# Optimization experiments

Hardware: AMD Instinct MI355X
Metric: run time of the kernel (lower is better)

The kernel has to match this reference:

```python
import jax, jax.numpy as jnp
import numpy as np

N_NODES = 100000
N_EDGES = 1600000
IN_CH = 1024
FEAT_CH = 128
OUT_CH = 3


def setup_inputs() -> dict:
    key = jax.random.key(0)
    ks = jax.random.split(key, 9)
    features = jax.random.normal(ks[0], (N_NODES, IN_CH), dtype=jnp.float32)
    edges = jax.random.randint(ks[1], (2, N_EDGES), 0, N_NODES, dtype=jnp.int64)
    edges2 = jax.random.randint(ks[2], (2, N_EDGES), 0, N_NODES, dtype=jnp.int64)
    edge_features = jax.random.normal(ks[3], (N_EDGES, 1), dtype=jnp.float32)
    additional_feature = jax.random.normal(ks[4], (N_NODES, 20), dtype=jnp.float32)
    # GCNConv linear weights (glorot-ish scale) and biases
    W1 = jax.random.normal(ks[5], (IN_CH, FEAT_CH), dtype=jnp.float32) * (1.0 / np.sqrt(IN_CH))
    b1 = jnp.zeros((FEAT_CH,), dtype=jnp.float32)
    W2 = jax.random.normal(ks[6], (FEAT_CH, OUT_CH), dtype=jnp.float32) * (1.0 / np.sqrt(FEAT_CH))
    b2 = jnp.zeros((OUT_CH,), dtype=jnp.float32)
    return {"features": features, "edges": edges, "edges2": edges2,
            "edge_features": edge_features, "additional_feature": additional_feature,
            "W1": W1, "b1": b1, "W2": W2, "b2": b2}


def gcn_conv(x, edge_index, W, b, num_nodes):
    """PyG GCNConv: x' = D^{-1/2}(A+I)D^{-1/2} x W + b (self-loops added)."""
    x = x @ W  # project first (cheaper feature dim for aggregation)
    loop = jnp.arange(num_nodes, dtype=edge_index.dtype)
    src = jnp.concatenate([edge_index[0], loop])
    dst = jnp.concatenate([edge_index[1], loop])
    deg = jax.ops.segment_sum(jnp.ones_like(dst, dtype=x.dtype), dst,
                              num_segments=num_nodes)  # >=1 due to self-loops
    dinv = jax.lax.rsqrt(deg)
    norm = dinv[src] * dinv[dst]  # [E+N]
    out = jax.ops.segment_sum(x[src] * norm[:, None], dst, num_segments=num_nodes)
    return out + b


def reference(features, edges, edges2, edge_features, additional_feature, W1, b1, W2, b2):
    # use_additional_channels=False -> features unchanged; edge_features forced to None
    n = features.shape[0]
    x = gcn_conv(features, edges2, W1, b1, n)
    x = jax.nn.relu(x)
    # dropout inactive in eval mode
    return gcn_conv(x, edges2, W2, b2, n)
```

## Files before the change

kernel.cpp:

```cpp
#include <hip/hip_runtime.h>
#include <hip/hip_bf16.h>

typedef __attribute__((ext_vector_type(8))) _Float16 half8;
typedef __attribute__((ext_vector_type(4))) float f32x4;

#define N_NODES 100000
#define N_EDGES 1600000
#define IN_CH 1024
#define FEAT 128
#define CAP 64
#define NDIG 196
#define CAPC 10240
#define NTILES ((N_NODES + 127) / 128)

__global__ void k_prep(const float* __restrict__ W1, _Float16* __restrict__ W1t,
                       int* __restrict__ cursorC, int* __restrict__ done) {
    int idx = blockIdx.x * 256 + threadIdx.x;
    if (idx < IN_CH * FEAT) {
        int col = idx & (FEAT - 1);
        int k = idx >> 7;
        W1t[(size_t)col * IN_CH + k] = (_Float16)W1[idx];
    }
    if (idx < NDIG) cursorC[idx] = idx * CAPC;
    if (idx == 0) *done = 0;
}

__global__ __launch_bounds__(256, 2) void k_build_gemm(
    const float* __restrict__ A, const _Float16* __restrict__ Bt,
    const int4* __restrict__ src4, const int4* __restrict__ dst4,
    int* __restrict__ cursorC, uint2* __restrict__ recs,
    int* __restrict__ csr, int* __restrict__ cnt, int* __restrict__ done,
    _Float16* __restrict__ H, int M, int e4)
{
    __shared__ union {
        _Float16 Bs[2][128][72];
        struct { int hist[NDIG], segoff[NDIG], lcur[NDIG]; } bin;
        int cl[512];
    } sm;
    const int t = threadIdx.x;

    if (blockIdx.x < NDIG) {
        const int b = blockIdx.x;
        if (t < NDIG) sm.bin.hist[t] = 0;
        __syncthreads();

        const int base4 = b * 2048;
        int4 sv[8], dv[8];
#pragma unroll
        for (int j = 0; j < 8; ++j) {
            int idx = base4 + j * 256 + t;
            if (idx < e4) { sv[j] = src4[idx]; dv[j] = dst4[idx]; }
            else { sv[j] = (int4){-1,-1,-1,-1}; dv[j] = (int4){-1,-1,-1,-1}; }
        }
#pragma unroll
        for (int j = 0; j < 8; ++j) {
            int dd[4] = {dv[j].x, dv[j].y, dv[j].z, dv[j].w};
            int ss[4] = {sv[j].x, sv[j].y, sv[j].z, sv[j].w};
#pragma unroll
            for (int c = 0; c < 4; ++c)
                if ((unsigned)dd[c] < N_NODES && (unsigned)ss[c] < N_NODES)
                    atomicAdd(&sm.bin.hist[dd[c] >> 9], 1);
        }
        __syncthreads();
        if (t < NDIG) {
            sm.bin.segoff[t] = atomicAdd(&cursorC[t], sm.bin.hist[t]);
            sm.bin.lcur[t] = 0;
        }
        __syncthreads();
#pragma unroll
        for (int j = 0; j < 8; ++j) {
            int dd[4] = {dv[j].x, dv[j].y, dv[j].z, dv[j].w};
            int ss[4] = {sv[j].x, sv[j].y, sv[j].z, sv[j].w};
#pragma unroll
            for (int c = 0; c < 4; ++c) {
                if ((unsigned)dd[c] < N_NODES && (unsigned)ss[c] < N_NODES) {
                    int dg = dd[c] >> 9;
                    int r = atomicAdd(&sm.bin.lcur[dg], 1);
                    int pos = sm.bin.segoff[dg] + r;
                    if (pos < (dg + 1) * CAPC)
                        recs[pos] = (uint2){(unsigned)ss[c], (unsigned)dd[c]};
                }
            }
        }
        __syncthreads();
        if (t == 0) {
            __threadfence();
            __hip_atomic_fetch_add(done, 1, __ATOMIC_RELEASE, __HIP_MEMORY_SCOPE_AGENT);
            while (__hip_atomic_load(done, __ATOMIC_ACQUIRE, __HIP_MEMORY_SCOPE_AGENT) < NDIG)
                __builtin_amdgcn_s_sleep(8);
        }
        __syncthreads();
        const int d = blockIdx.x;
        for (int j = t; j < 512; j += 256) sm.cl[j] = 0;
        __syncthreads();
        const int base = d * CAPC;
        int n = cursorC[d] - base;
        if (n > CAPC) n = CAPC;
        for (int k = t; k < n; k += 256) {
            uint2 r = recs[base + k];
            int local = (int)r.y & 511;
            int slot = atomicAdd(&sm.cl[local], 1);
            if (slot < CAP) csr[((int)r.y << 6) + slot] = (int)r.x;
        }
        __syncthreads();
        const int node0 = d << 9;
        for (int j = t; j < 512; j += 256) {
            int node = node0 + j;
            if (node < N_NODES) cnt[node] = sm.cl[j] < CAP ? sm.cl[j] : CAP;
        }
        return;
    }

    const int wid = t >> 6, lane = t & 63;
    const int brow0 = (blockIdx.x - NDIG) * 128;
    const int NKT = IN_CH / 64;

    f32x4 acc[2][8];
#pragma unroll
    for (int m = 0; m < 2; ++m)
#pragma unroll
        for (int nn = 0; nn < 8; ++nn) acc[m][nn] = (f32x4){0.f, 0.f, 0.f, 0.f};

    int r0 = brow0 + wid * 32 + (lane & 15);
    int r1 = r0 + 16;
    if (r0 >= M) r0 = M - 1;
    if (r1 >= M) r1 = M - 1;
    const int kbase = (lane >> 4) * 8;
    const float* pa0 = A + (size_t)r0 * IN_CH + kbase;
    const float* pa1 = A + (size_t)r1 * IN_CH + kbase;
    const int bcol = t >> 1;
    const int bko = (t & 1) * 32;
    const _Float16* pb = Bt + (size_t)bcol * IN_CH + bko;

    float4 ar[2][2][2];
    half8 af[2][2];
    half8 bst[4];

#define LOAD_A(kt)                                                              \
    {                                                                           \
        _Pragma("unroll") for (int m = 0; m < 2; ++m) {                         \
            const float* p_ = (m ? pa1 : pa0) + (kt) * 64;                      \
            _Pragma("unroll") for (int kk = 0; kk < 2; ++kk) {                  \
                ar[m][kk][0] = *(const float4*)(p_ + kk * 32);                  \
                ar[m][kk][1] = *(const float4*)(p_ + kk * 32 + 4);              \
            }                                                                   \
        }                                                                       \
    }
#define CVT_A()                                                                 \
    {                                                                           \
        _Pragma("unroll") for (int m = 0; m < 2; ++m)                           \
        _Pragma("unroll") for (int kk = 0; kk < 2; ++kk) {                      \
            half8 h;                                                            \
            h[0] = (_Float16)ar[m][kk][0].x; h[1] = (_Float16)ar[m][kk][0].y;   \
            h[2] = (_Float16)ar[m][kk][0].z; h[3] = (_Float16)ar[m][kk][0].w;   \
            h[4] = (_Float16)ar[m][kk][1].x; h[5] = (_Float16)ar[m][kk][1].y;   \
            h[6] = (_Float16)ar[m][kk][1].z; h[7] = (_Float16)ar[m][kk][1].w;   \
            af[m][kk] = h;                                                      \
        }                                                                       \
    }
#define LOAD_B(kt)                                                              \
    {                                                                           \
        const half8* s_ = (const half8*)(pb + (kt) * 64);                       \
        _Pragma("unroll") for (int j = 0; j < 4; ++j) bst[j] = s_[j];           \
    }
#define WRITE_B(buf)                                                            \
    {                                                                           \
        _Pragma("unroll") for (int j = 0; j < 4; ++j)                           \
            *(half8*)(&sm.Bs[buf][bcol][bko + j * 8]) = bst[j];                 \
    }

    LOAD_A(0); LOAD_B(0);
    CVT_A();
    WRITE_B(0);
    __syncthreads();

    for (int kt = 0; kt < NKT; ++kt) {
        const int cur = kt & 1;
        const bool more = (kt + 1 < NKT);
        if (more) { LOAD_B(kt + 1); LOAD_A(kt + 1); }
#pragma unroll
        for (int kk = 0; kk < 2; ++kk) {
            half8 a0 = af[0][kk], a1 = af[1][kk];
#pragma unroll
            for (int nn = 0; nn < 8; ++nn) {
                half8 bb = *(const half8*)(&sm.Bs[cur][nn * 16 + (lane & 15)][kk * 32 + kbase]);
                acc[0][nn] = __builtin_amdgcn_mfma_f32_16x16x32_f16(a0, bb, acc[0][nn], 0, 0, 0);
                acc[1][nn] = __builtin_amdgcn_mfma_f32_16x16x32_f16(a1, bb, acc[1][nn], 0, 0, 0);
            }
        }
        if (more) {
            CVT_A();
            WRITE_B(cur ^ 1);
            __syncthreads();
        }
    }
#undef LOAD_A
#undef CVT_A
#undef LOAD_B
#undef WRITE_B

    int colb = lane & 15, rgrp = (lane >> 4) * 4;
#pragma unroll
    for (int m = 0; m < 2; ++m) {
#pragma unroll
        for (int r = 0; r < 4; ++r) {
            int grow = brow0 + wid * 32 + m * 16 + rgrp + r;
            if (grow < M) {
                _Float16* hp = H + (size_t)grow * FEAT + colb;
#pragma unroll
                for (int nn = 0; nn < 8; ++nn) hp[nn * 16] = (_Float16)acc[m][nn][r];
            }
        }
    }
}

__device__ __forceinline__ float dinv_of(const int* cnt, int i, int& m) {
    m = cnt[i];
    return rsqrtf((float)(m + 1));
}

__global__ __launch_bounds__(256) void k_agg1(const _Float16* __restrict__ H,
                                              const int* __restrict__ csr,
                                              const int* __restrict__ cnt,
                                              const float* __restrict__ b1,
                                              const float* __restrict__ W2,
                                              float* __restrict__ Y, int n) {
    int wid = threadIdx.x >> 6, lane = threadIdx.x & 63;
    int i = blockIdx.x * 4 + wid;
    if (i >= n) return;
    const int g = lane >> 4, u = lane & 15;
    int m;
    float di = dinv_of(cnt, i, m);
    int base = i << 6;

    int sl; float dl;
    if (lane < m) {
        sl = csr[base + lane];
        int cs = cnt[sl];
        dl = rsqrtf((float)(cs + 1));
    } else {
        sl = i;
        dl = (lane == m) ? di : 0.f;
    }
    int mm = (m < 63 ? m : 63) + 1;

    float ax[8];
#pragma unroll
    for (int j = 0; j < 8; ++j) ax[j] = 0.f;

    for (int e = 0; e < mm; e += 8) {
        int i0 = e + g, i1 = e + 4 + g;
        bool v0 = i0 < mm, v1 = i1 < mm;
        int c0i = v0 ? i0 : 0, c1i = v1 ? i1 : 0;
        int s0 = __shfl(sl, c0i);
        float w0 = __shfl(dl, c0i);
        int s1 = __shfl(sl, c1i);
        float w1 = __shfl(dl, c1i);
        if (!v0) { s0 = i; w0 = 0.f; }
        if (!v1) { s1 = i; w1 = 0.f; }
        half8 h0 = *(const half8*)(H + ((size_t)s0 << 7) + u * 8);
        half8 h1 = *(const half8*)(H + ((size_t)s1 << 7) + u * 8);
#pragma unroll
        for (int j = 0; j < 8; ++j) ax[j] += w0 * (float)h0[j] + w1 * (float)h1[j];
    }

#pragma unroll
    for (int j = 0; j < 8; ++j) {
        ax[j] += __shfl_xor(ax[j], 16);
        ax[j] += __shfl_xor(ax[j], 32);
    }

    int c0 = u * 8;
    float y0 = 0.f, y1 = 0.f, y2 = 0.f;
#pragma unroll
    for (int j = 0; j < 8; ++j) {
        float x = di * ax[j] + b1[c0 + j];
        x = x > 0.f ? x : 0.f;
        y0 += x * W2[(c0 + j) * 3 + 0];
        y1 += x * W2[(c0 + j) * 3 + 1];
        y2 += x * W2[(c0 + j) * 3 + 2];
    }
#pragma unroll
    for (int d = 1; d < 16; d <<= 1) {
        y0 += __shfl_xor(y0, d);
        y1 += __shfl_xor(y1, d);
        y2 += __shfl_xor(y2, d);
    }
    if (lane == 0) {
        float* yp = Y + (size_t)i * 4;
        yp[0] = di * y0; yp[1] = di * y1; yp[2] = di * y2;
    }
}

__global__ void k_agg2(const float* __restrict__ Y, const int* __restrict__ csr,
                       const int* __restrict__ cnt, const float* __restrict__ b2,
                       float* __restrict__ out, int n) {
    int i = blockIdx.x * 256 + threadIdx.x;
    if (i >= n) return;
    int m;
    float di = dinv_of(cnt, i, m);
    int base = i << 6;
    const float4* Y4 = (const float4*)Y;
    float4 self = Y4[i];
    float a0 = self.x, a1 = self.y, a2 = self.z;
    int e = 0;
    for (; e + 1 < m; e += 2) {
        int s0 = csr[base + e], s1 = csr[base + e + 1];
        float4 v0 = Y4[s0], v1 = Y4[s1];
        a0 += v0.x + v1.x;
        a1 += v0.y + v1.y;
        a2 += v0.z + v1.z;
    }
    if (e < m) {
        float4 v0 = Y4[csr[base + e]];
        a0 += v0.x; a1 += v0.y; a2 += v0.z;
    }
    out[(size_t)i * 3 + 0] = di * a0 + b2[0];
    out[(size_t)i * 3 + 1] = di * a1 + b2[1];
    out[(size_t)i * 3 + 2] = di * a2 + b2[2];
}

extern "C" void kernel_launch(void* const* d_in, const int* in_sizes, int n_in,
                              void* d_out, int out_size, void* d_ws, size_t ws_size,
                              hipStream_t stream) {
    const float* features = (const float*)d_in[0];
    const int* edges2 = (const int*)d_in[2];
    const float* W1 = (const float*)d_in[5];
    const float* b1 = (const float*)d_in[6];
    const float* W2 = (const float*)d_in[7];
    const float* b2 = (const float*)d_in[8];
    float* out = (float*)d_out;

    const int N = N_NODES, E = N_EDGES;
    const int* srcp = edges2;
    const int* dstp = edges2 + E;

    char* p = (char*)d_ws;
    auto carve = [&](size_t bytes) { char* q = p; p += (bytes + 255) & ~(size_t)255; return q; };
    int* cnt      = (int*)carve(4 * (size_t)N);
    int* cursorC  = (int*)carve(4 * NDIG);
    int* done     = (int*)carve(4);
    uint2* recs   = (uint2*)carve(8 * (size_t)NDIG * CAPC);
    int* csr      = (int*)carve(4 * (size_t)N * CAP);
    _Float16* W1t = (_Float16*)carve(2 * (size_t)IN_CH * FEAT);
    _Float16* H   = (_Float16*)carve(2 * (size_t)N * FEAT);
    float* Y      = (float*)carve(16 * (size_t)N);

    k_prep<<<dim3(512), dim3(256), 0, stream>>>(W1, W1t, cursorC, done);
    k_build_gemm<<<dim3(NDIG + NTILES), dim3(256), 0, stream>>>(
        features, W1t, (const int4*)srcp, (const int4*)dstp,
        cursorC, recs, csr, cnt, done, H, N, E / 4);
    k_agg1<<<dim3((N + 3) / 4), dim3(256), 0, stream>>>(H, csr, cnt, b1, W2, Y, N);
    k_agg2<<<dim3((N + 255) / 256), dim3(256), 0, stream>>>(Y, csr, cnt, b2, out, N);
}
```

Before: 269.5 us.

## Fuse all stages into one persistent cooperative kernel with grid syncs

Merges weight prep, CSR build, GEMM, and both aggregation stages into one cooperative persistent kernel. Stages are separated by grid.sync, and GEMM tiles are handed out through an atomic tile counter. Each agg1 wave prefetches the next node's count and neighbor list. This is meant to remove the overhead of four kernel launches and the gaps between them. The cost is that the grid is capped at 512 resident blocks, so the GEMM and aggregation run with fewer workers and pay for grid-wide barriers.

```diff
diff --git a/kernel.cpp b/kernel.cpp
--- a/kernel.cpp
+++ b/kernel.cpp
@@ -1,5 +1,8 @@
 #include <hip/hip_runtime.h>
 #include <hip/hip_bf16.h>
+#include <hip/hip_cooperative_groups.h>
+
+namespace cg = cooperative_groups;
 
 typedef __attribute__((ext_vector_type(8))) _Float16 half8;
 typedef __attribute__((ext_vector_type(4))) float f32x4;
@@ -13,12 +16,351 @@
 #define CAPC 10240
 #define NTILES ((N_NODES + 127) / 128)
 
+template <typename LDS>
+__device__ __forceinline__ void gemm_tile(LDS* Bs, const float* __restrict__ A,
+                                          const _Float16* __restrict__ Bt,
+                                          _Float16* __restrict__ H, int M,
+                                          int tile, int t) {
+    const int wid = t >> 6, lane = t & 63;
+    const int brow0 = tile * 128;
+    const int NKT = IN_CH / 64;
+
+    f32x4 acc[2][8];
+#pragma unroll
+    for (int m = 0; m < 2; ++m)
+#pragma unroll
+        for (int nn = 0; nn < 8; ++nn) acc[m][nn] = (f32x4){0.f, 0.f, 0.f, 0.f};
+
+    int r0 = brow0 + wid * 32 + (lane & 15);
+    int r1 = r0 + 16;
+    if (r0 >= M) r0 = M - 1;
+    if (r1 >= M) r1 = M - 1;
+    const int kbase = (lane >> 4) * 8;
+    const float* pa0 = A + (size_t)r0 * IN_CH + kbase;
+    const float* pa1 = A + (size_t)r1 * IN_CH + kbase;
+    const int bcol = t >> 1;
+    const int bko = (t & 1) * 32;
+    const _Float16* pb = Bt + (size_t)bcol * IN_CH + bko;
+
+    float4 ar[2][2][2];
+    half8 af[2][2];
+    half8 bst[4];
+
+#define LOAD_A(kt)                                                              \
+    {                                                                           \
+        _Pragma("unroll") for (int m = 0; m < 2; ++m) {                         \
+            const float* p_ = (m ? pa1 : pa0) + (kt) * 64;                      \
+            _Pragma("unroll") for (int kk = 0; kk < 2; ++kk) {                  \
+                ar[m][kk][0] = *(const float4*)(p_ + kk * 32);                  \
+                ar[m][kk][1] = *(const float4*)(p_ + kk * 32 + 4);              \
+            }                                                                   \
+        }                                                                       \
+    }
+#define CVT_A()                                                                 \
+    {                                                                           \
+        _Pragma("unroll") for (int m = 0; m < 2; ++m)                           \
+        _Pragma("unroll") for (int kk = 0; kk < 2; ++kk) {                      \
+            half8 h;                                                            \
+            h[0] = (_Float16)ar[m][kk][0].x; h[1] = (_Float16)ar[m][kk][0].y;   \
+            h[2] = (_Float16)ar[m][kk][0].z; h[3] = (_Float16)ar[m][kk][0].w;   \
+            h[4] = (_Float16)ar[m][kk][1].x; h[5] = (_Float16)ar[m][kk][1].y;   \
+            h[6] = (_Float16)ar[m][kk][1].z; h[7] = (_Float16)ar[m][kk][1].w;   \
+            af[m][kk] = h;                                                      \
+        }                                                                       \
+    }
+#define LOAD_B(kt)                                                              \
+    {                                                                           \
+        const half8* s_ = (const half8*)(pb + (kt) * 64);                       \
+        _Pragma("unroll") for (int j = 0; j < 4; ++j) bst[j] = s_[j];           \
+    }
+#define WRITE_B(buf)                                                            \
+    {                                                                           \
+        _Pragma("unroll") for (int j = 0; j < 4; ++j)                           \
+            *(half8*)(&(*Bs)[buf][bcol][bko + j * 8]) = bst[j];                 \
+    }
+
+    LOAD_A(0); LOAD_B(0);
+    CVT_A();
+    WRITE_B(0);
+    __syncthreads();
+
+    for (int kt = 0; kt < NKT; ++kt) {
+        const int cur = kt & 1;
+        const bool more = (kt + 1 < NKT);
+        if (more) { LOAD_B(kt + 1); LOAD_A(kt + 1); }
+#pragma unroll
+        for (int kk = 0; kk < 2; ++kk) {
+            half8 a0 = af[0][kk], a1 = af[1][kk];
+#pragma unroll
+            for (int nn = 0; nn < 8; ++nn) {
+                half8 bb = *(const half8*)(&(*Bs)[cur][nn * 16 + (lane & 15)][kk * 32 + kbase]);
+                acc[0][nn] = __builtin_amdgcn_mfma_f32_16x16x32_f16(a0, bb, acc[0][nn], 0, 0, 0);
+                acc[1][nn] = __builtin_amdgcn_mfma_f32_16x16x32_f16(a1, bb, acc[1][nn], 0, 0, 0);
+            }
+        }
+        if (more) {
+            CVT_A();
+            WRITE_B(cur ^ 1);
+            __syncthreads();
+        }
+    }
+#undef LOAD_A
+#undef CVT_A
+#undef LOAD_B
+#undef WRITE_B
+
+    int colb = lane & 15, rgrp = (lane >> 4) * 4;
+#pragma unroll
+    for (int m = 0; m < 2; ++m) {
+#pragma unroll
+        for (int r = 0; r < 4; ++r) {
+            int grow = brow0 + wid * 32 + m * 16 + rgrp + r;
+            if (grow < M) {
+                _Float16* hp = H + (size_t)grow * FEAT + colb;
+#pragma unroll
+                for (int nn = 0; nn < 8; ++nn) hp[nn * 16] = (_Float16)acc[m][nn][r];
+            }
+        }
+    }
+}
+
+__device__ __forceinline__ void agg1_node(const _Float16* __restrict__ H,
+                                          const int* __restrict__ cnt,
+                                          const float* __restrict__ b1,
+                                          const float* __restrict__ W2,
+                                          float* __restrict__ Y,
+                                          int i, int lane, int m, int sl_raw) {
+    const int g = lane >> 4, u = lane & 15;
+    float di = rsqrtf((float)(m + 1));
+    int sl; float dl;
+    if (lane < m) {
+        sl = sl_raw;
+        int cs = cnt[sl];
+        dl = rsqrtf((float)(cs + 1));
+    } else {
+        sl = i;
+        dl = (lane == m) ? di : 0.f;
+    }
+    int mm = (m < 63 ? m : 63) + 1;
+
+    float ax[8];
+#pragma unroll
+    for (int j = 0; j < 8; ++j) ax[j] = 0.f;
+
+    for (int e = 0; e < mm; e += 8) {
+        int i0 = e + g, i1 = e + 4 + g;
+        bool v0 = i0 < mm, v1 = i1 < mm;
+        int c0i = v0 ? i0 : 0, c1i = v1 ? i1 : 0;
+        int s0 = __shfl(sl, c0i);
+        float w0 = __shfl(dl, c0i);
+        int s1 = __shfl(sl, c1i);
+        float w1 = __shfl(dl, c1i);
+        if (!v0) { s0 = i; w0 = 0.f; }
+        if (!v1) { s1 = i; w1 = 0.f; }
+        half8 h0 = *(const half8*)(H + ((size_t)s0 << 7) + u * 8);
+        half8 h1 = *(const half8*)(H + ((size_t)s1 << 7) + u * 8);
+#pragma unroll
+        for (int j = 0; j < 8; ++j) ax[j] += w0 * (float)h0[j] + w1 * (float)h1[j];
+    }
+
+#pragma unroll
+    for (int j = 0; j < 8; ++j) {
+        ax[j] += __shfl_xor(ax[j], 16);
+        ax[j] += __shfl_xor(ax[j], 32);
+    }
+
+    int c0 = u * 8;
+    float y0 = 0.f, y1 = 0.f, y2 = 0.f;
+#pragma unroll
+    for (int j = 0; j < 8; ++j) {
+        float x = di * ax[j] + b1[c0 + j];
+        x = x > 0.f ? x : 0.f;
+        y0 += x * W2[(c0 + j) * 3 + 0];
+        y1 += x * W2[(c0 + j) * 3 + 1];
+        y2 += x * W2[(c0 + j) * 3 + 2];
+    }
+#pragma unroll
+    for (int d = 1; d < 16; d <<= 1) {
+        y0 += __shfl_xor(y0, d);
+        y1 += __shfl_xor(y1, d);
+        y2 += __shfl_xor(y2, d);
+    }
+    if (lane == 0) {
+        float* yp = Y + (size_t)i * 4;
+        yp[0] = di * y0; yp[1] = di * y1; yp[2] = di * y2;
+    }
+}
+
+__device__ __forceinline__ void agg2_node(const float* __restrict__ Y,
+                                          const int* __restrict__ csr,
+                                          const int* __restrict__ cnt,
+                                          const float* __restrict__ b2,
+                                          float* __restrict__ out, int i) {
+    int m = cnt[i];
+    float di = rsqrtf((float)(m + 1));
+    int base = i << 6;
+    const float4* Y4 = (const float4*)Y;
+    float4 self = Y4[i];
+    float a0 = self.x, a1 = self.y, a2 = self.z;
+    int e = 0;
+    for (; e + 1 < m; e += 2) {
+        int s0 = csr[base + e], s1 = csr[base + e + 1];
+        float4 v0 = Y4[s0], v1 = Y4[s1];
+        a0 += v0.x + v1.x;
+        a1 += v0.y + v1.y;
+        a2 += v0.z + v1.z;
+    }
+    if (e < m) {
+        float4 v0 = Y4[csr[base + e]];
+        a0 += v0.x; a1 += v0.y; a2 += v0.z;
+    }
+    out[(size_t)i * 3 + 0] = di * a0 + b2[0];
+    out[(size_t)i * 3 + 1] = di * a1 + b2[1];
+    out[(size_t)i * 3 + 2] = di * a2 + b2[2];
+}
+
+__global__ __launch_bounds__(256, 2) void k_mega(
+    const float* __restrict__ A, const float* __restrict__ W1,
+    const int4* __restrict__ src4, const int4* __restrict__ dst4,
+    const float* __restrict__ b1, const float* __restrict__ W2,
+    const float* __restrict__ b2, float* __restrict__ out,
+    int* __restrict__ cursorC, uint2* __restrict__ recs,
+    int* __restrict__ csr, int* __restrict__ cnt,
+    int* __restrict__ done, int* __restrict__ tilectr,
+    _Float16* __restrict__ W1t, _Float16* __restrict__ H,
+    float* __restrict__ Y, int e4)
+{
+    cg::grid_group grid = cg::this_grid();
+    __shared__ union {
+        _Float16 Bs[2][128][72];
+        struct { int hist[NDIG], segoff[NDIG], lcur[NDIG]; } bin;
+        int cl[512];
+    } sm;
+    const int t = threadIdx.x;
+    const int b = blockIdx.x;
+    const int nb = gridDim.x;
+    const int gtid = b * 256 + t;
+    const int nthr = nb * 256;
+
+    for (int idx = gtid; idx < IN_CH * FEAT; idx += nthr) {
+        int col = idx & (FEAT - 1), k = idx >> 7;
+        W1t[(size_t)col * IN_CH + k] = (_Float16)W1[idx];
+    }
+    if (gtid < NDIG) cursorC[gtid] = gtid * CAPC;
+    if (gtid == 0) { *done = 0; *tilectr = 0; }
+    grid.sync();
+
+    if (b < NDIG) {
+        if (t < NDIG) sm.bin.hist[t] = 0;
+        __syncthreads();
+        const int base4 = b * 2048;
+        int4 sv[8], dv[8];
+#pragma unroll
+        for (int j = 0; j < 8; ++j) {
+            int idx = base4 + j * 256 + t;
+            if (idx < e4) { sv[j] = src4[idx]; dv[j] = dst4[idx]; }
+            else { sv[j] = (int4){-1,-1,-1,-1}; dv[j] = (int4){-1,-1,-1,-1}; }
+        }
+#pragma unroll
+        for (int j = 0; j < 8; ++j) {
+            int dd[4] = {dv[j].x, dv[j].y, dv[j].z, dv[j].w};
+            int ss[4] = {sv[j].x, sv[j].y, sv[j].z, sv[j].w};
+#pragma unroll
+            for (int c = 0; c < 4; ++c)
+                if ((unsigned)dd[c] < N_NODES && (unsigned)ss[c] < N_NODES)
+                    atomicAdd(&sm.bin.hist[dd[c] >> 9], 1);
+        }
+        __syncthreads();
+        if (t < NDIG) {
+            sm.bin.segoff[t] = atomicAdd(&cursorC[t], sm.bin.hist[t]);
+            sm.bin.lcur[t] = 0;
+        }
+        __syncthreads();
+#pragma unroll
+        for (int j = 0; j < 8; ++j) {
+            int dd[4] = {dv[j].x, dv[j].y, dv[j].z, dv[j].w};
+            int ss[4] = {sv[j].x, sv[j].y, sv[j].z, sv[j].w};
+#pragma unroll
+            for (int c = 0; c < 4; ++c) {
+                if ((unsigned)dd[c] < N_NODES && (unsigned)ss[c] < N_NODES) {
+                    int dg = dd[c] >> 9;
+                    int r = atomicAdd(&sm.bin.lcur[dg], 1);
+                    int pos = sm.bin.segoff[dg] + r;
+                    if (pos < (dg + 1) * CAPC)
+                        recs[pos] = (uint2){(unsigned)ss[c], (unsigned)dd[c]};
+                }
+            }
+        }
+        __syncthreads();
+        if (t == 0) {
+            __threadfence();
+            __hip_atomic_fetch_add(done, 1, __ATOMIC_RELEASE, __HIP_MEMORY_SCOPE_AGENT);
+            while (__hip_atomic_load(done, __ATOMIC_ACQUIRE, __HIP_MEMORY_SCOPE_AGENT) < NDIG)
+                __builtin_amdgcn_s_sleep(8);
+        }
+        __syncthreads();
+        for (int j = t; j < 512; j += 256) sm.cl[j] = 0;
+        __syncthreads();
+        const int base = b * CAPC;
+        int n = cursorC[b] - base;
+        if (n > CAPC) n = CAPC;
+        for (int k = t; k < n; k += 256) {
+            uint2 r = recs[base + k];
+            int local = (int)r.y & 511;
+            int slot = atomicAdd(&sm.cl[local], 1);
+            if (slot < CAP) csr[((int)r.y << 6) + slot] = (int)r.x;
+        }
+        __syncthreads();
+        const int node0 = b << 9;
+        for (int j = t; j < 512; j += 256) {
+            int node = node0 + j;
+            if (node < N_NODES) cnt[node] = sm.cl[j] < CAP ? sm.cl[j] : CAP;
+        }
+    }
+    {
+        __shared__ int tsh;
+        for (;;) {
+            __syncthreads();
+            if (t == 0) tsh = atomicAdd(tilectr, 1);
+            __syncthreads();
+            int tile = tsh;
+            if (tile >= NTILES) break;
+            gemm_tile(&sm.Bs, A, W1t, H, N_NODES, tile, t);
+        }
+    }
+    grid.sync();
+
+    {
+        const int wid = t >> 6, lane = t & 63;
+        const int stride = nb * 4;
+        int i = b * 4 + wid;
+        int m_cur = 0, sl_cur = 0;
+        if (i < N_NODES) {
+            m_cur = cnt[i];
+            sl_cur = csr[(i << 6) + lane];
+        }
+        for (; i < N_NODES; ) {
+            int inext = i + stride;
+            int m_pf = 0, sl_pf = 0;
+            if (inext < N_NODES) {
+                m_pf = cnt[inext];
+                sl_pf = csr[(inext << 6) + lane];
+            }
+            agg1_node(H, cnt, b1, W2, Y, i, lane, m_cur, sl_cur);
+            i = inext; m_cur = m_pf; sl_cur = sl_pf;
+        }
+    }
+    grid.sync();
+
+    for (int i = gtid; i < N_NODES; i += nthr)
+        agg2_node(Y, csr, cnt, b2, out, i);
+}
+
 __global__ void k_prep(const float* __restrict__ W1, _Float16* __restrict__ W1t,
                        int* __restrict__ cursorC, int* __restrict__ done) {
     int idx = blockIdx.x * 256 + threadIdx.x;
     if (idx < IN_CH * FEAT) {
-        int col = idx & (FEAT - 1);
-        int k = idx >> 7;
+        int col = idx & (FEAT - 1), k = idx >> 7;
         W1t[(size_t)col * IN_CH + k] = (_Float16)W1[idx];
     }
     if (idx < NDIG) cursorC[idx] = idx * CAPC;
@@ -43,7 +385,6 @@
         const int b = blockIdx.x;
         if (t < NDIG) sm.bin.hist[t] = 0;
         __syncthreads();
-
         const int base4 = b * 2048;
         int4 sv[8], dv[8];
 #pragma unroll
@@ -90,11 +431,10 @@
                 __builtin_amdgcn_s_sleep(8);
         }
         __syncthreads();
-        const int d = blockIdx.x;
         for (int j = t; j < 512; j += 256) sm.cl[j] = 0;
         __syncthreads();
-        const int base = d * CAPC;
-        int n = cursorC[d] - base;
+        const int base = blockIdx.x * CAPC;
+        int n = cursorC[blockIdx.x] - base;
         if (n > CAPC) n = CAPC;
         for (int k = t; k < n; k += 256) {
             uint2 r = recs[base + k];
@@ -103,120 +443,14 @@
             if (slot < CAP) csr[((int)r.y << 6) + slot] = (int)r.x;
         }
         __syncthreads();
-        const int node0 = d << 9;
+        const int node0 = blockIdx.x << 9;
         for (int j = t; j < 512; j += 256) {
             int node = node0 + j;
             if (node < N_NODES) cnt[node] = sm.cl[j] < CAP ? sm.cl[j] : CAP;
         }
         return;
     }
-
-    const int wid = t >> 6, lane = t & 63;
-    const int brow0 = (blockIdx.x - NDIG) * 128;
-    const int NKT = IN_CH / 64;
-
-    f32x4 acc[2][8];
-#pragma unroll
-    for (int m = 0; m < 2; ++m)
-#pragma unroll
-        for (int nn = 0; nn < 8; ++nn) acc[m][nn] = (f32x4){0.f, 0.f, 0.f, 0.f};
-
-    int r0 = brow0 + wid * 32 + (lane & 15);
-    int r1 = r0 + 16;
-    if (r0 >= M) r0 = M - 1;
-    if (r1 >= M) r1 = M - 1;
-    const int kbase = (lane >> 4) * 8;
-    const float* pa0 = A + (size_t)r0 * IN_CH + kbase;
-    const float* pa1 = A + (size_t)r1 * IN_CH + kbase;
-    const int bcol = t >> 1;
-    const int bko = (t & 1) * 32;
-    const _Float16* pb = Bt + (size_t)bcol * IN_CH + bko;
-
-    float4 ar[2][2][2];
-    half8 af[2][2];
-    half8 bst[4];
-
-#define LOAD_A(kt)                                                              \
-    {                                                                           \
-        _Pragma("unroll") for (int m = 0; m < 2; ++m) {                         \
-            const float* p_ = (m ? pa1 : pa0) + (kt) * 64;                      \
-            _Pragma("unroll") for (int kk = 0; kk < 2; ++kk) {                  \
-                ar[m][kk][0] = *(const float4*)(p_ + kk * 32);                  \
-                ar[m][kk][1] = *(const float4*)(p_ + kk * 32 + 4);              \
-            }                                                                   \
-        }                                                                       \
-    }
-#define CVT_A()                                                                 \
-    {                                                                           \
-        _Pragma("unroll") for (int m = 0; m < 2; ++m)                           \
-        _Pragma("unroll") for (int kk = 0; kk < 2; ++kk) {                      \
-            half8 h;                                                            \
-            h[0] = (_Float16)ar[m][kk][0].x; h[1] = (_Float16)ar[m][kk][0].y;   \
-            h[2] = (_Float16)ar[m][kk][0].z; h[3] = (_Float16)ar[m][kk][0].w;   \
-            h[4] = (_Float16)ar[m][kk][1].x; h[5] = (_Float16)ar[m][kk][1].y;   \
-            h[6] = (_Float16)ar[m][kk][1].z; h[7] = (_Float16)ar[m][kk][1].w;   \
-            af[m][kk] = h;                                                      \
-        }                                                                       \
-    }
-#define LOAD_B(kt)                                                              \
-    {                                                                           \
-        const half8* s_ = (const half8*)(pb + (kt) * 64);                       \
-        _Pragma("unroll") for (int j = 0; j < 4; ++j) bst[j] = s_[j];           \
-    }
-#define WRITE_B(buf)                                                            \
-    {                                                                           \
-        _Pragma("unroll") for (int j = 0; j < 4; ++j)                           \
-            *(half8*)(&sm.Bs[buf][bcol][bko + j * 8]) = bst[j];                 \
-    }
-
-    LOAD_A(0); LOAD_B(0);
-    CVT_A();
-    WRITE_B(0);
-    __syncthreads();
-
-    for (int kt = 0; kt < NKT; ++kt) {
-        const int cur = kt & 1;
-        const bool more = (kt + 1 < NKT);
-        if (more) { LOAD_B(kt + 1); LOAD_A(kt + 1); }
-#pragma unroll
-        for (int kk = 0; kk < 2; ++kk) {
-            half8 a0 = af[0][kk], a1 = af[1][kk];
-#pragma unroll
-            for (int nn = 0; nn < 8; ++nn) {
-                half8 bb = *(const half8*)(&sm.Bs[cur][nn * 16 + (lane & 15)][kk * 32 + kbase]);
-                acc[0][nn] = __builtin_amdgcn_mfma_f32_16x16x32_f16(a0, bb, acc[0][nn], 0, 0, 0);
-                acc[1][nn] = __builtin_amdgcn_mfma_f32_16x16x32_f16(a1, bb, acc[1][nn], 0, 0, 0);
-            }
-        }
-        if (more) {
-            CVT_A();
-            WRITE_B(cur ^ 1);
-            __syncthreads();
-        }
-    }
-#undef LOAD_A
-#undef CVT_A
-#undef LOAD_B
-#undef WRITE_B
-
-    int colb = lane & 15, rgrp = (lane >> 4) * 4;
-#pragma unroll
-    for (int m = 0; m < 2; ++m) {
-#pragma unroll
-        for (int r = 0; r < 4; ++r) {
-            int grow = brow0 + wid * 32 + m * 16 + rgrp + r;
-            if (grow < M) {
-                _Float16* hp = H + (size_t)grow * FEAT + colb;
-#pragma unroll
-                for (int nn = 0; nn < 8; ++nn) hp[nn * 16] = (_Float16)acc[m][nn][r];
-            }
-        }
-    }
-}
-
-__device__ __forceinline__ float dinv_of(const int* cnt, int i, int& m) {
-    m = cnt[i];
-    return rsqrtf((float)(m + 1));
+    gemm_tile(&sm.Bs, A, Bt, H, M, blockIdx.x - NDIG, t);
 }
 
 __global__ __launch_bounds__(256) void k_agg1(const _Float16* __restrict__ H,
@@ -228,68 +462,9 @@
     int wid = threadIdx.x >> 6, lane = threadIdx.x & 63;
     int i = blockIdx.x * 4 + wid;
     if (i >= n) return;
-    const int g = lane >> 4, u = lane & 15;
-    int m;
-    float di = dinv_of(cnt, i, m);
-    int base = i << 6;
-
-    int sl; float dl;
-    if (lane < m) {
-        sl = csr[base + lane];
-        int cs = cnt[sl];
-        dl = rsqrtf((float)(cs + 1));
-    } else {
-        sl = i;
-        dl = (lane == m) ? di : 0.f;
-    }
-    int mm = (m < 63 ? m : 63) + 1;
-
-    float ax[8];
-#pragma unroll
-    for (int j = 0; j < 8; ++j) ax[j] = 0.f;
-
-    for (int e = 0; e < mm; e += 8) {
-        int i0 = e + g, i1 = e + 4 + g;
-        bool v0 = i0 < mm, v1 = i1 < mm;
-        int c0i = v0 ? i0 : 0, c1i = v1 ? i1 : 0;
-        int s0 = __shfl(sl, c0i);
-        float w0 = __shfl(dl, c0i);
-        int s1 = __shfl(sl, c1i);
-        float w1 = __shfl(dl, c1i);
-        if (!v0) { s0 = i; w0 = 0.f; }
-        if (!v1) { s1 = i; w1 = 0.f; }
-        half8 h0 = *(const half8*)(H + ((size_t)s0 << 7) + u * 8);
-        half8 h1 = *(const half8*)(H + ((size_t)s1 << 7) + u * 8);
-#pragma unroll
-        for (int j = 0; j < 8; ++j) ax[j] += w0 * (float)h0[j] + w1 * (float)h1[j];
-    }
-
-#pragma unroll
-    for (int j = 0; j < 8; ++j) {
-        ax[j] += __shfl_xor(ax[j], 16);
-        ax[j] += __shfl_xor(ax[j], 32);
-    }
-
-    int c0 = u * 8;
-    float y0 = 0.f, y1 = 0.f, y2 = 0.f;
-#pragma unroll
-    for (int j = 0; j < 8; ++j) {
-        float x = di * ax[j] + b1[c0 + j];
-        x = x > 0.f ? x : 0.f;
-        y0 += x * W2[(c0 + j) * 3 + 0];
-        y1 += x * W2[(c0 + j) * 3 + 1];
-        y2 += x * W2[(c0 + j) * 3 + 2];
-    }
-#pragma unroll
-    for (int d = 1; d < 16; d <<= 1) {
-        y0 += __shfl_xor(y0, d);
-        y1 += __shfl_xor(y1, d);
-        y2 += __shfl_xor(y2, d);
-    }
-    if (lane == 0) {
-        float* yp = Y + (size_t)i * 4;
-        yp[0] = di * y0; yp[1] = di * y1; yp[2] = di * y2;
-    }
+    int m = cnt[i];
+    int sl_raw = (lane < m) ? csr[(i << 6) + lane] : 0;
+    agg1_node(H, cnt, b1, W2, Y, i, lane, m, sl_raw);
 }
 
 __global__ void k_agg2(const float* __restrict__ Y, const int* __restrict__ csr,
@@ -297,27 +472,7 @@
                        float* __restrict__ out, int n) {
     int i = blockIdx.x * 256 + threadIdx.x;
     if (i >= n) return;
-    int m;
-    float di = dinv_of(cnt, i, m);
-    int base = i << 6;
-    const float4* Y4 = (const float4*)Y;
-    float4 self = Y4[i];
-    float a0 = self.x, a1 = self.y, a2 = self.z;
-    int e = 0;
-    for (; e + 1 < m; e += 2) {
-        int s0 = csr[base + e], s1 = csr[base + e + 1];
-        float4 v0 = Y4[s0], v1 = Y4[s1];
-        a0 += v0.x + v1.x;
-        a1 += v0.y + v1.y;
-        a2 += v0.z + v1.z;
-    }
-    if (e < m) {
-        float4 v0 = Y4[csr[base + e]];
-        a0 += v0.x; a1 += v0.y; a2 += v0.z;
-    }
-    out[(size_t)i * 3 + 0] = di * a0 + b2[0];
-    out[(size_t)i * 3 + 1] = di * a1 + b2[1];
-    out[(size_t)i * 3 + 2] = di * a2 + b2[2];
+    agg2_node(Y, csr, cnt, b2, out, i);
 }
 
 extern "C" void kernel_launch(void* const* d_in, const int* in_sizes, int n_in,
@@ -334,22 +489,43 @@
     const int N = N_NODES, E = N_EDGES;
     const int* srcp = edges2;
     const int* dstp = edges2 + E;
+    const int4* src4 = (const int4*)srcp;
+    const int4* dst4 = (const int4*)dstp;
+    int e4 = E / 4;
 
     char* p = (char*)d_ws;
     auto carve = [&](size_t bytes) { char* q = p; p += (bytes + 255) & ~(size_t)255; return q; };
     int* cnt      = (int*)carve(4 * (size_t)N);
     int* cursorC  = (int*)carve(4 * NDIG);
     int* done     = (int*)carve(4);
+    int* tilectr  = (int*)carve(4);
     uint2* recs   = (uint2*)carve(8 * (size_t)NDIG * CAPC);
     int* csr      = (int*)carve(4 * (size_t)N * CAP);
     _Float16* W1t = (_Float16*)carve(2 * (size_t)IN_CH * FEAT);
     _Float16* H   = (_Float16*)carve(2 * (size_t)N * FEAT);
     float* Y      = (float*)carve(16 * (size_t)N);
 
+    int dev = 0, ncu = 0, maxb = 0;
+    bool coop_ok = (hipGetDevice(&dev) == hipSuccess) &&
+                   (hipDeviceGetAttribute(&ncu, hipDeviceAttributeMultiprocessorCount, dev) == hipSuccess) &&
+                   (hipOccupancyMaxActiveBlocksPerMultiprocessor(&maxb, k_mega, 256, 0) == hipSuccess) &&
+                   maxb >= 1 && ncu >= 1;
+    int grid = coop_ok ? maxb * ncu : 0;
+    if (grid > 512) grid = 512;
+    if (coop_ok && grid >= NDIG + 4) {
+        void* args[] = {(void*)&features, (void*)&W1, (void*)&src4, (void*)&dst4,
+                        (void*)&b1, (void*)&W2, (void*)&b2, (void*)&out,
+                        (void*)&cursorC, (void*)&recs, (void*)&csr, (void*)&cnt,
+                        (void*)&done, (void*)&tilectr, (void*)&W1t, (void*)&H,
+                        (void*)&Y, (void*)&e4};
+        hipError_t le = hipLaunchCooperativeKernel(k_mega, dim3(grid), dim3(256),
+                                                   args, 0, stream);
+        if (le == hipSuccess) return;
+    }
+
     k_prep<<<dim3(512), dim3(256), 0, stream>>>(W1, W1t, cursorC, done);
     k_build_gemm<<<dim3(NDIG + NTILES), dim3(256), 0, stream>>>(
-        features, W1t, (const int4*)srcp, (const int4*)dstp,
-        cursorC, recs, csr, cnt, done, H, N, E / 4);
+        features, W1t, src4, dst4, cursorC, recs, csr, cnt, done, H, N, e4);
     k_agg1<<<dim3((N + 3) / 4), dim3(256), 0, stream>>>(H, csr, cnt, b1, W2, Y, N);
     k_agg2<<<dim3((N + 255) / 256), dim3(256), 0, stream>>>(Y, csr, cnt, b2, out, N);
 }
```

Result: slower. 541.1 us (+100.8%).
